# Kernel tuning notes

Measured on AMD Instinct MI355X. Metric: run time of the kernel, lower is better.

Reference implementation:

```python
import jax, jax.numpy as jnp
import numpy as np

X_SIZE, Y_SIZE, C_SIZE, H = 4, 2, 3, 128
B, C_CTX, T = 4, 512, 512


def _xavier(key, shape):
    fan_in, fan_out = shape[0], shape[1]
    a = jnp.sqrt(6.0 / (fan_in + fan_out))
    return jax.random.uniform(key, shape, jnp.float32, -a, a)


def setup_inputs() -> dict:
    key = jax.random.key(0)
    ks = jax.random.split(key, 9)
    return {
        "context_x": jax.random.normal(ks[0], (B, C_CTX, X_SIZE), jnp.float32),
        "context_y": jax.random.normal(ks[1], (B, C_CTX, Y_SIZE), jnp.float32),
        "target_x": jax.random.normal(ks[2], (B, T, X_SIZE), jnp.float32),
        "W_in": _xavier(ks[3], (C_SIZE + Y_SIZE, H)),
        "b_in": jnp.zeros((H,), jnp.float32),
        "W_ctx": _xavier(ks[4], (C_SIZE, H)),
        "b_ctx": jnp.zeros((H,), jnp.float32),
        "W_tgt": _xavier(ks[5], (H, H)),
        "b_tgt": jnp.zeros((H,), jnp.float32),
    }


def reference(context_x, context_y, target_x, W_in, b_in, W_ctx, b_ctx, W_tgt, b_tgt):
    ctx_c = context_x[..., :C_SIZE]                         # [B, C, c]
    # value: projected concat of context coords + context values
    enc_in = jnp.concatenate([ctx_c, context_y], axis=-1)   # [B, C, c+y]
    value = enc_in @ W_in + b_in                            # [B, C, H]
    key_ = ctx_c @ W_ctx + b_ctx                            # [B, C, H]
    query = target_x[..., :C_SIZE] @ W_ctx + b_ctx          # [B, T, H]
    # L1-distance attention scores: -sum_h |0.5*(key - query)|
    diff = (key_[:, None, :, :] - query[:, :, None, :]) * 0.5  # [B, T, C, H]
    scores = -jnp.sum(jnp.abs(diff), axis=-1)               # [B, T, C]
    w = jax.nn.softmax(scores, axis=-1)                     # [B, T, C]
    rep = jnp.einsum('btc,bch->bth', w, value)              # [B, T, H]
    return rep @ W_tgt + b_tgt
```

## Files before the change

### kernel.cpp

```cpp
#include <hip/hip_runtime.h>

#define BB 4
#define CC 512
#define TDIM 512
#define HH 128
#define TT 4
#define CHK 128
#define NCHK 4

__global__ __launch_bounds__(128) void prep_kernel(
    const float* __restrict__ ctx_x, const float* __restrict__ ctx_y,
    const float* __restrict__ tgt_x,
    const float* __restrict__ W_in, const float* __restrict__ b_in,
    const float* __restrict__ W_ctx, const float* __restrict__ b_ctx,
    float* __restrict__ key, float* __restrict__ query, float* __restrict__ value)
{
    int row = blockIdx.x;
    int h   = threadIdx.x;

    float4 cx = ((const float4*)ctx_x)[row];
    float2 cy = ((const float2*)ctx_y)[row];
    float4 tx = ((const float4*)tgt_x)[row];

    float wi0 = W_in[0*HH+h], wi1 = W_in[1*HH+h], wi2 = W_in[2*HH+h];
    float wi3 = W_in[3*HH+h], wi4 = W_in[4*HH+h];
    float wc0 = W_ctx[0*HH+h], wc1 = W_ctx[1*HH+h], wc2 = W_ctx[2*HH+h];
    float bi  = b_in[h], bc = b_ctx[h];

    value[row*HH+h] = fmaf(cx.x,wi0, fmaf(cx.y,wi1, fmaf(cx.z,wi2, fmaf(cy.x,wi3, fmaf(cy.y,wi4, bi)))));
    key  [row*HH+h] = fmaf(cx.x,wc0, fmaf(cx.y,wc1, fmaf(cx.z,wc2, bc)));
    query[row*HH+h] = fmaf(tx.x,wc0, fmaf(tx.y,wc1, fmaf(tx.z,wc2, bc)));
}

__global__ __launch_bounds__(256) void fused_kernel(
    const float* __restrict__ key, const float* __restrict__ query,
    const float* __restrict__ value, const float* __restrict__ W_tgt,
    const float* __restrict__ b_tgt, float* __restrict__ out)
{
    const int bx   = blockIdx.x;
    const int b    = bx >> 7;
    const int t0   = (bx & 127) * TT;
    const int tid  = threadIdx.x;
    const int g    = tid >> 6;
    const int lane = tid & 63;

    __shared__ __align__(16) float s[2][TT][CHK];
    __shared__ __align__(16) float pT[2][CHK][TT];
    __shared__ __align__(16) float fct[2][TT];
    __shared__ __align__(16) float linv[TT];
    __shared__ __align__(16) float partial[8][TT][HH];
    __shared__ __align__(16) float rep[TT][HH];

    const int cq = tid >> 3;
    const int hq = tid & 7;
    float4 qr[TT][4];
    #pragma unroll
    for (int t = 0; t < TT; ++t)
        #pragma unroll
        for (int j = 0; j < 4; ++j)
            qr[t][j] = *(const float4*)&query[(b*TDIM + t0 + t)*HH + j*32 + hq*4];

    const int cs = lane >> 5;
    const int hv = lane & 31;
    float4 acc[TT];
    #pragma unroll
    for (int t = 0; t < TT; ++t) acc[t] = make_float4(0.f,0.f,0.f,0.f);
    float m_run = -1e30f, l_run = 0.f;

    auto SCORE = [&](int ch, int p) {
        const float* kp = &key[(b*CC + ch*CHK + cq*4)*HH];
        float a0[TT], a1[TT], a2[TT], a3[TT];
        #pragma unroll
        for (int t = 0; t < TT; ++t) { a0[t]=0.f; a1[t]=0.f; a2[t]=0.f; a3[t]=0.f; }
        #pragma unroll
        for (int j = 0; j < 4; ++j) {
            const int hb = j*32 + hq*4;
            float4 k0 = *(const float4*)(kp + 0*HH + hb);
            float4 k1 = *(const float4*)(kp + 1*HH + hb);
            float4 k2 = *(const float4*)(kp + 2*HH + hb);
            float4 k3 = *(const float4*)(kp + 3*HH + hb);
            #pragma unroll
            for (int t = 0; t < TT; ++t) {
                float4 qv = qr[t][j];
                a0[t] += fabsf(k0.x-qv.x)+fabsf(k0.y-qv.y)+fabsf(k0.z-qv.z)+fabsf(k0.w-qv.w);
                a1[t] += fabsf(k1.x-qv.x)+fabsf(k1.y-qv.y)+fabsf(k1.z-qv.z)+fabsf(k1.w-qv.w);
                a2[t] += fabsf(k2.x-qv.x)+fabsf(k2.y-qv.y)+fabsf(k2.z-qv.z)+fabsf(k2.w-qv.w);
                a3[t] += fabsf(k3.x-qv.x)+fabsf(k3.y-qv.y)+fabsf(k3.z-qv.z)+fabsf(k3.w-qv.w);
            }
        }
        #pragma unroll
        for (int t = 0; t < TT; ++t) {
            float v0=a0[t], v1=a1[t], v2=a2[t], v3=a3[t];
            v0 += __shfl_xor(v0,1); v0 += __shfl_xor(v0,2); v0 += __shfl_xor(v0,4);
            v1 += __shfl_xor(v1,1); v1 += __shfl_xor(v1,2); v1 += __shfl_xor(v1,4);
            v2 += __shfl_xor(v2,1); v2 += __shfl_xor(v2,2); v2 += __shfl_xor(v2,4);
            v3 += __shfl_xor(v3,1); v3 += __shfl_xor(v3,2); v3 += __shfl_xor(v3,4);
            if (hq == 0)
                *(float4*)&s[p][t][cq*4] =
                    make_float4(-0.5f*v0, -0.5f*v1, -0.5f*v2, -0.5f*v3);
        }
    };

    auto SOFTMAX = [&](int p) {
        float x0 = s[p][g][lane], x1 = s[p][g][lane+64];
        float mc = fmaxf(x0, x1);
        #pragma unroll
        for (int msk = 32; msk; msk >>= 1) mc = fmaxf(mc, __shfl_xor(mc, msk));
        float m_new = fmaxf(m_run, mc);
        float e0 = __expf(x0 - m_new), e1 = __expf(x1 - m_new);
        float sum = e0 + e1;
        #pragma unroll
        for (int msk = 32; msk; msk >>= 1) sum += __shfl_xor(sum, msk);
        float f = __expf(m_run - m_new);
        l_run = fmaf(l_run, f, sum);
        m_run = m_new;
        pT[p][lane   ][g] = e0;
        pT[p][lane+64][g] = e1;
        if (lane == 0) fct[p][g] = f;
    };

    auto PV = [&](int ch, int p) {
        const float4 fv = *(const float4*)&fct[p][0];
        acc[0].x*=fv.x; acc[0].y*=fv.x; acc[0].z*=fv.x; acc[0].w*=fv.x;
        acc[1].x*=fv.y; acc[1].y*=fv.y; acc[1].z*=fv.y; acc[1].w*=fv.y;
        acc[2].x*=fv.z; acc[2].y*=fv.z; acc[2].z*=fv.z; acc[2].w*=fv.z;
        acc[3].x*=fv.w; acc[3].y*=fv.w; acc[3].z*=fv.w; acc[3].w*=fv.w;
        const int cbase = g*32 + cs*16;
        const float* vp = &value[(b*CC + ch*CHK + cbase)*HH + hv*4];
        #pragma unroll 4
        for (int c = 0; c < 16; ++c) {
            float4 p4 = *(const float4*)&pT[p][cbase + c][0];
            float4 vv = *(const float4*)(vp + c*HH);
            acc[0].x=fmaf(p4.x,vv.x,acc[0].x); acc[0].y=fmaf(p4.x,vv.y,acc[0].y);
            acc[0].z=fmaf(p4.x,vv.z,acc[0].z); acc[0].w=fmaf(p4.x,vv.w,acc[0].w);
            acc[1].x=fmaf(p4.y,vv.x,acc[1].x); acc[1].y=fmaf(p4.y,vv.y,acc[1].y);
            acc[1].z=fmaf(p4.y,vv.z,acc[1].z); acc[1].w=fmaf(p4.y,vv.w,acc[1].w);
            acc[2].x=fmaf(p4.z,vv.x,acc[2].x); acc[2].y=fmaf(p4.z,vv.y,acc[2].y);
            acc[2].z=fmaf(p4.z,vv.z,acc[2].z); acc[2].w=fmaf(p4.z,vv.w,acc[2].w);
            acc[3].x=fmaf(p4.w,vv.x,acc[3].x); acc[3].y=fmaf(p4.w,vv.y,acc[3].y);
            acc[3].z=fmaf(p4.w,vv.z,acc[3].z); acc[3].w=fmaf(p4.w,vv.w,acc[3].w);
        }
    };

    SCORE(0, 0);
    __syncthreads();
    SOFTMAX(0);
    __syncthreads();
    SCORE(1, 1);  PV(0, 0);
    __syncthreads();
    SOFTMAX(1);
    __syncthreads();
    SCORE(2, 0);  PV(1, 1);
    __syncthreads();
    SOFTMAX(0);
    __syncthreads();
    SCORE(3, 1);  PV(2, 0);
    __syncthreads();
    SOFTMAX(1);
    __syncthreads();
    PV(3, 1);

    if (lane == 0) linv[g] = 1.f / l_run;
    #pragma unroll
    for (int t = 0; t < TT; ++t)
        *(float4*)&partial[g*2 + cs][t][hv*4] = acc[t];
    __syncthreads();

    for (int i = tid; i < TT*HH; i += 256) {
        const int t = i >> 7, h = i & 127;
        float r = 0.f;
        #pragma unroll
        for (int gg = 0; gg < 8; ++gg) r += partial[gg][t][h];
        rep[t][h] = r * linv[t];
    }
    __syncthreads();

    {
        const int lt = tid >> 7, h = tid & 127;
        float o0 = b_tgt[h], o1 = o0;
        for (int k = 0; k < HH; k += 4) {
            float4 r0 = *(const float4*)&rep[lt    ][k];
            float4 r1 = *(const float4*)&rep[lt + 2][k];
            float w0 = W_tgt[(k+0)*HH + h];
            float w1 = W_tgt[(k+1)*HH + h];
            float w2 = W_tgt[(k+2)*HH + h];
            float w3 = W_tgt[(k+3)*HH + h];
            o0 = fmaf(r0.x,w0, fmaf(r0.y,w1, fmaf(r0.z,w2, fmaf(r0.w,w3, o0))));
            o1 = fmaf(r1.x,w0, fmaf(r1.y,w1, fmaf(r1.z,w2, fmaf(r1.w,w3, o1))));
        }
        out[(b*TDIM + t0 + lt    )*HH + h] = o0;
        out[(b*TDIM + t0 + lt + 2)*HH + h] = o1;
    }
}

extern "C" void kernel_launch(void* const* d_in, const int* in_sizes, int n_in,
                              void* d_out, int out_size, void* d_ws, size_t ws_size,
                              hipStream_t stream) {
    const float* ctx_x = (const float*)d_in[0];
    const float* ctx_y = (const float*)d_in[1];
    const float* tgt_x = (const float*)d_in[2];
    const float* W_in  = (const float*)d_in[3];
    const float* b_in  = (const float*)d_in[4];
    const float* W_ctx = (const float*)d_in[5];
    const float* b_ctx = (const float*)d_in[6];
    const float* W_tgt = (const float*)d_in[7];
    const float* b_tgt = (const float*)d_in[8];

    float* ws    = (float*)d_ws;
    float* key   = ws;
    float* query = ws + 1*BB*CC*HH;
    float* value = ws + 2*BB*CC*HH;

    prep_kernel<<<BB*CC, 128, 0, stream>>>(ctx_x, ctx_y, tgt_x,
                                           W_in, b_in, W_ctx, b_ctx,
                                           key, query, value);
    fused_kernel<<<BB*(TDIM/TT), 256, 0, stream>>>(key, query, value,
                                                   W_tgt, b_tgt, (float*)d_out);
}
```

Baseline: 35.98 us.

## Double fused attention block to 512 threads with halved per-thread work

```diff
diff --git a/kernel.cpp b/kernel.cpp
--- a/kernel.cpp
+++ b/kernel.cpp
@@ -32,7 +32,7 @@
     query[row*HH+h] = fmaf(tx.x,wc0, fmaf(tx.y,wc1, fmaf(tx.z,wc2, bc)));
 }
 
-__global__ __launch_bounds__(256) void fused_kernel(
+__global__ __launch_bounds__(512, 4) void fused_kernel(
     const float* __restrict__ key, const float* __restrict__ query,
     const float* __restrict__ value, const float* __restrict__ W_tgt,
     const float* __restrict__ b_tgt, float* __restrict__ out)
@@ -41,7 +41,7 @@
     const int b    = bx >> 7;
     const int t0   = (bx & 127) * TT;
     const int tid  = threadIdx.x;
-    const int g    = tid >> 6;
+    const int wave = tid >> 6;
     const int lane = tid & 63;
 
     __shared__ __align__(16) float s[2][TT][CHK];
@@ -51,20 +51,18 @@
     __shared__ __align__(16) float partial[8][TT][HH];
     __shared__ __align__(16) float rep[TT][HH];
 
-    const int cq = tid >> 3;
-    const int hq = tid & 7;
-    float4 qr[TT][4];
+    const int cq = tid >> 4;
+    const int hq = tid & 15;
+    float2 qr[TT][4];
     #pragma unroll
     for (int t = 0; t < TT; ++t)
         #pragma unroll
         for (int j = 0; j < 4; ++j)
-            qr[t][j] = *(const float4*)&query[(b*TDIM + t0 + t)*HH + j*32 + hq*4];
-
-    const int cs = lane >> 5;
-    const int hv = lane & 31;
-    float4 acc[TT];
+            qr[t][j] = *(const float2*)&query[(b*TDIM + t0 + t)*HH + j*32 + hq*2];
+
+    float2 acc[TT];
     #pragma unroll
-    for (int t = 0; t < TT; ++t) acc[t] = make_float4(0.f,0.f,0.f,0.f);
+    for (int t = 0; t < TT; ++t) acc[t] = make_float2(0.f, 0.f);
     float m_run = -1e30f, l_run = 0.f;
 
     auto SCORE = [&](int ch, int p) {
@@ -74,27 +72,27 @@
         for (int t = 0; t < TT; ++t) { a0[t]=0.f; a1[t]=0.f; a2[t]=0.f; a3[t]=0.f; }
         #pragma unroll
         for (int j = 0; j < 4; ++j) {
-            const int hb = j*32 + hq*4;
-            float4 k0 = *(const float4*)(kp + 0*HH + hb);
-            float4 k1 = *(const float4*)(kp + 1*HH + hb);
-            float4 k2 = *(const float4*)(kp + 2*HH + hb);
-            float4 k3 = *(const float4*)(kp + 3*HH + hb);
+            const int hb = j*32 + hq*2;
+            float2 k0 = *(const float2*)(kp + 0*HH + hb);
+            float2 k1 = *(const float2*)(kp + 1*HH + hb);
+            float2 k2 = *(const float2*)(kp + 2*HH + hb);
+            float2 k3 = *(const float2*)(kp + 3*HH + hb);
             #pragma unroll
             for (int t = 0; t < TT; ++t) {
-                float4 qv = qr[t][j];
-                a0[t] += fabsf(k0.x-qv.x)+fabsf(k0.y-qv.y)+fabsf(k0.z-qv.z)+fabsf(k0.w-qv.w);
-                a1[t] += fabsf(k1.x-qv.x)+fabsf(k1.y-qv.y)+fabsf(k1.z-qv.z)+fabsf(k1.w-qv.w);
-                a2[t] += fabsf(k2.x-qv.x)+fabsf(k2.y-qv.y)+fabsf(k2.z-qv.z)+fabsf(k2.w-qv.w);
-                a3[t] += fabsf(k3.x-qv.x)+fabsf(k3.y-qv.y)+fabsf(k3.z-qv.z)+fabsf(k3.w-qv.w);
+                float2 qv = qr[t][j];
+                a0[t] += fabsf(k0.x-qv.x) + fabsf(k0.y-qv.y);
+                a1[t] += fabsf(k1.x-qv.x) + fabsf(k1.y-qv.y);
+                a2[t] += fabsf(k2.x-qv.x) + fabsf(k2.y-qv.y);
+                a3[t] += fabsf(k3.x-qv.x) + fabsf(k3.y-qv.y);
             }
         }
         #pragma unroll
         for (int t = 0; t < TT; ++t) {
             float v0=a0[t], v1=a1[t], v2=a2[t], v3=a3[t];
-            v0 += __shfl_xor(v0,1); v0 += __shfl_xor(v0,2); v0 += __shfl_xor(v0,4);
-            v1 += __shfl_xor(v1,1); v1 += __shfl_xor(v1,2); v1 += __shfl_xor(v1,4);
-            v2 += __shfl_xor(v2,1); v2 += __shfl_xor(v2,2); v2 += __shfl_xor(v2,4);
-            v3 += __shfl_xor(v3,1); v3 += __shfl_xor(v3,2); v3 += __shfl_xor(v3,4);
+            v0 += __shfl_xor(v0,1); v0 += __shfl_xor(v0,2); v0 += __shfl_xor(v0,4); v0 += __shfl_xor(v0,8);
+            v1 += __shfl_xor(v1,1); v1 += __shfl_xor(v1,2); v1 += __shfl_xor(v1,4); v1 += __shfl_xor(v1,8);
+            v2 += __shfl_xor(v2,1); v2 += __shfl_xor(v2,2); v2 += __shfl_xor(v2,4); v2 += __shfl_xor(v2,8);
+            v3 += __shfl_xor(v3,1); v3 += __shfl_xor(v3,2); v3 += __shfl_xor(v3,4); v3 += __shfl_xor(v3,8);
             if (hq == 0)
                 *(float4*)&s[p][t][cq*4] =
                     make_float4(-0.5f*v0, -0.5f*v1, -0.5f*v2, -0.5f*v3);
@@ -102,7 +100,7 @@
     };
 
     auto SOFTMAX = [&](int p) {
-        float x0 = s[p][g][lane], x1 = s[p][g][lane+64];
+        float x0 = s[p][wave][lane], x1 = s[p][wave][lane+64];
         float mc = fmaxf(x0, x1);
         #pragma unroll
         for (int msk = 32; msk; msk >>= 1) mc = fmaxf(mc, __shfl_xor(mc, msk));
@@ -114,60 +112,56 @@
         float f = __expf(m_run - m_new);
         l_run = fmaf(l_run, f, sum);
         m_run = m_new;
-        pT[p][lane   ][g] = e0;
-        pT[p][lane+64][g] = e1;
-        if (lane == 0) fct[p][g] = f;
+        pT[p][lane   ][wave] = e0;
+        pT[p][lane+64][wave] = e1;
+        if (lane == 0) fct[p][wave] = f;
     };
 
     auto PV = [&](int ch, int p) {
         const float4 fv = *(const float4*)&fct[p][0];
-        acc[0].x*=fv.x; acc[0].y*=fv.x; acc[0].z*=fv.x; acc[0].w*=fv.x;
-        acc[1].x*=fv.y; acc[1].y*=fv.y; acc[1].z*=fv.y; acc[1].w*=fv.y;
-        acc[2].x*=fv.z; acc[2].y*=fv.z; acc[2].z*=fv.z; acc[2].w*=fv.z;
-        acc[3].x*=fv.w; acc[3].y*=fv.w; acc[3].z*=fv.w; acc[3].w*=fv.w;
-        const int cbase = g*32 + cs*16;
-        const float* vp = &value[(b*CC + ch*CHK + cbase)*HH + hv*4];
+        acc[0].x *= fv.x; acc[0].y *= fv.x;
+        acc[1].x *= fv.y; acc[1].y *= fv.y;
+        acc[2].x *= fv.z; acc[2].y *= fv.z;
+        acc[3].x *= fv.w; acc[3].y *= fv.w;
+        const int cbase = wave * 16;
+        const float* vp = &value[(b*CC + ch*CHK + cbase)*HH + lane*2];
         #pragma unroll 4
         for (int c = 0; c < 16; ++c) {
             float4 p4 = *(const float4*)&pT[p][cbase + c][0];
-            float4 vv = *(const float4*)(vp + c*HH);
-            acc[0].x=fmaf(p4.x,vv.x,acc[0].x); acc[0].y=fmaf(p4.x,vv.y,acc[0].y);
-            acc[0].z=fmaf(p4.x,vv.z,acc[0].z); acc[0].w=fmaf(p4.x,vv.w,acc[0].w);
-            acc[1].x=fmaf(p4.y,vv.x,acc[1].x); acc[1].y=fmaf(p4.y,vv.y,acc[1].y);
-            acc[1].z=fmaf(p4.y,vv.z,acc[1].z); acc[1].w=fmaf(p4.y,vv.w,acc[1].w);
-            acc[2].x=fmaf(p4.z,vv.x,acc[2].x); acc[2].y=fmaf(p4.z,vv.y,acc[2].y);
-            acc[2].z=fmaf(p4.z,vv.z,acc[2].z); acc[2].w=fmaf(p4.z,vv.w,acc[2].w);
-            acc[3].x=fmaf(p4.w,vv.x,acc[3].x); acc[3].y=fmaf(p4.w,vv.y,acc[3].y);
-            acc[3].z=fmaf(p4.w,vv.z,acc[3].z); acc[3].w=fmaf(p4.w,vv.w,acc[3].w);
+            float2 vv = *(const float2*)(vp + c*HH);
+            acc[0].x = fmaf(p4.x, vv.x, acc[0].x); acc[0].y = fmaf(p4.x, vv.y, acc[0].y);
+            acc[1].x = fmaf(p4.y, vv.x, acc[1].x); acc[1].y = fmaf(p4.y, vv.y, acc[1].y);
+            acc[2].x = fmaf(p4.z, vv.x, acc[2].x); acc[2].y = fmaf(p4.z, vv.y, acc[2].y);
+            acc[3].x = fmaf(p4.w, vv.x, acc[3].x); acc[3].y = fmaf(p4.w, vv.y, acc[3].y);
         }
     };
 
     SCORE(0, 0);
     __syncthreads();
-    SOFTMAX(0);
+    if (wave < 4) SOFTMAX(0);
     __syncthreads();
     SCORE(1, 1);  PV(0, 0);
     __syncthreads();
-    SOFTMAX(1);
+    if (wave < 4) SOFTMAX(1);
     __syncthreads();
     SCORE(2, 0);  PV(1, 1);
     __syncthreads();
-    SOFTMAX(0);
+    if (wave < 4) SOFTMAX(0);
     __syncthreads();
     SCORE(3, 1);  PV(2, 0);
     __syncthreads();
-    SOFTMAX(1);
+    if (wave < 4) SOFTMAX(1);
     __syncthreads();
     PV(3, 1);
 
-    if (lane == 0) linv[g] = 1.f / l_run;
+    if (wave < 4 && lane == 0) linv[wave] = 1.f / l_run;
     #pragma unroll
     for (int t = 0; t < TT; ++t)
-        *(float4*)&partial[g*2 + cs][t][hv*4] = acc[t];
-    __syncthreads();
-
-    for (int i = tid; i < TT*HH; i += 256) {
-        const int t = i >> 7, h = i & 127;
+        *(float2*)&partial[wave][t][lane*2] = acc[t];
+    __syncthreads();
+
+    {
+        const int t = tid >> 7, h = tid & 127;
         float r = 0.f;
         #pragma unroll
         for (int gg = 0; gg < 8; ++gg) r += partial[gg][t][h];
@@ -177,19 +171,16 @@
 
     {
         const int lt = tid >> 7, h = tid & 127;
-        float o0 = b_tgt[h], o1 = o0;
+        float o = b_tgt[h];
         for (int k = 0; k < HH; k += 4) {
-            float4 r0 = *(const float4*)&rep[lt    ][k];
-            float4 r1 = *(const float4*)&rep[lt + 2][k];
+            float4 r0 = *(const float4*)&rep[lt][k];
             float w0 = W_tgt[(k+0)*HH + h];
             float w1 = W_tgt[(k+1)*HH + h];
             float w2 = W_tgt[(k+2)*HH + h];
             float w3 = W_tgt[(k+3)*HH + h];
-            o0 = fmaf(r0.x,w0, fmaf(r0.y,w1, fmaf(r0.z,w2, fmaf(r0.w,w3, o0))));
-            o1 = fmaf(r1.x,w0, fmaf(r1.y,w1, fmaf(r1.z,w2, fmaf(r1.w,w3, o1))));
-        }
-        out[(b*TDIM + t0 + lt    )*HH + h] = o0;
-        out[(b*TDIM + t0 + lt + 2)*HH + h] = o1;
+            o = fmaf(r0.x,w0, fmaf(r0.y,w1, fmaf(r0.z,w2, fmaf(r0.w,w3, o))));
+        }
+        out[(b*TDIM + t0 + lt)*HH + h] = o;
     }
 }
 
@@ -214,6 +205,6 @@
     prep_kernel<<<BB*CC, 128, 0, stream>>>(ctx_x, ctx_y, tgt_x,
                                            W_in, b_in, W_ctx, b_ctx,
                                            key, query, value);
-    fused_kernel<<<BB*(TDIM/TT), 256, 0, stream>>>(key, query, value,
+    fused_kernel<<<BB*(TDIM/TT), 512, 0, stream>>>(key, query, value,
                                                    W_tgt, b_tgt, (float*)d_out);
 }
```

Result: slower. 48.01 us (+33.4%).

## Split context across waves with per-wave online softmax and final merge

Applied to the files above, without the earlier changes.

```diff
diff --git a/kernel.cpp b/kernel.cpp
--- a/kernel.cpp
+++ b/kernel.cpp
@@ -5,8 +5,10 @@
 #define TDIM 512
 #define HH 128
 #define TT 4
-#define CHK 128
-#define NCHK 4
+#define NW 4
+#define CPW 128
+#define SC 32
+#define NSC 4
 
 __global__ __launch_bounds__(128) void prep_kernel(
     const float* __restrict__ ctx_x, const float* __restrict__ ctx_y,
@@ -41,18 +43,18 @@
     const int b    = bx >> 7;
     const int t0   = (bx & 127) * TT;
     const int tid  = threadIdx.x;
-    const int g    = tid >> 6;
+    const int wv   = tid >> 6;
     const int lane = tid & 63;
 
-    __shared__ __align__(16) float s[2][TT][CHK];
-    __shared__ __align__(16) float pT[2][CHK][TT];
-    __shared__ __align__(16) float fct[2][TT];
-    __shared__ __align__(16) float linv[TT];
-    __shared__ __align__(16) float partial[8][TT][HH];
+    __shared__ __align__(16) float s_w[NW][TT][SC];
+    __shared__ __align__(16) float pT_w[NW][SC][TT];
+    __shared__ __align__(16) float f_w[NW][TT];
+    __shared__ __align__(16) float2 ml_w[NW][TT];
+    __shared__ __align__(16) float partial[NW][TT][HH];
     __shared__ __align__(16) float rep[TT][HH];
 
-    const int cq = tid >> 3;
-    const int hq = tid & 7;
+    const int cl = lane >> 3;
+    const int hq = lane & 7;
     float4 qr[TT][4];
     #pragma unroll
     for (int t = 0; t < TT; ++t)
@@ -60,118 +62,123 @@
         for (int j = 0; j < 4; ++j)
             qr[t][j] = *(const float4*)&query[(b*TDIM + t0 + t)*HH + j*32 + hq*4];
 
+    const int tg = lane >> 4;
+    const int ci = lane & 15;
     const int cs = lane >> 5;
     const int hv = lane & 31;
+
     float4 acc[TT];
     #pragma unroll
     for (int t = 0; t < TT; ++t) acc[t] = make_float4(0.f,0.f,0.f,0.f);
     float m_run = -1e30f, l_run = 0.f;
 
-    auto SCORE = [&](int ch, int p) {
-        const float* kp = &key[(b*CC + ch*CHK + cq*4)*HH];
-        float a0[TT], a1[TT], a2[TT], a3[TT];
-        #pragma unroll
-        for (int t = 0; t < TT; ++t) { a0[t]=0.f; a1[t]=0.f; a2[t]=0.f; a3[t]=0.f; }
-        #pragma unroll
-        for (int j = 0; j < 4; ++j) {
-            const int hb = j*32 + hq*4;
-            float4 k0 = *(const float4*)(kp + 0*HH + hb);
-            float4 k1 = *(const float4*)(kp + 1*HH + hb);
-            float4 k2 = *(const float4*)(kp + 2*HH + hb);
-            float4 k3 = *(const float4*)(kp + 3*HH + hb);
+    #pragma unroll 1
+    for (int scix = 0; scix < NSC; ++scix) {
+        const int cbase = wv*CPW + scix*SC;
+
+        {
+            const float* kp = &key[(b*CC + cbase + cl*4)*HH];
+            float a0[TT], a1[TT], a2[TT], a3[TT];
+            #pragma unroll
+            for (int t = 0; t < TT; ++t) { a0[t]=0.f; a1[t]=0.f; a2[t]=0.f; a3[t]=0.f; }
+            #pragma unroll
+            for (int j = 0; j < 4; ++j) {
+                const int hb = j*32 + hq*4;
+                float4 k0 = *(const float4*)(kp + 0*HH + hb);
+                float4 k1 = *(const float4*)(kp + 1*HH + hb);
+                float4 k2 = *(const float4*)(kp + 2*HH + hb);
+                float4 k3 = *(const float4*)(kp + 3*HH + hb);
+                #pragma unroll
+                for (int t = 0; t < TT; ++t) {
+                    float4 qv = qr[t][j];
+                    a0[t] += fabsf(k0.x-qv.x)+fabsf(k0.y-qv.y)+fabsf(k0.z-qv.z)+fabsf(k0.w-qv.w);
+                    a1[t] += fabsf(k1.x-qv.x)+fabsf(k1.y-qv.y)+fabsf(k1.z-qv.z)+fabsf(k1.w-qv.w);
+                    a2[t] += fabsf(k2.x-qv.x)+fabsf(k2.y-qv.y)+fabsf(k2.z-qv.z)+fabsf(k2.w-qv.w);
+                    a3[t] += fabsf(k3.x-qv.x)+fabsf(k3.y-qv.y)+fabsf(k3.z-qv.z)+fabsf(k3.w-qv.w);
+                }
+            }
             #pragma unroll
             for (int t = 0; t < TT; ++t) {
-                float4 qv = qr[t][j];
-                a0[t] += fabsf(k0.x-qv.x)+fabsf(k0.y-qv.y)+fabsf(k0.z-qv.z)+fabsf(k0.w-qv.w);
-                a1[t] += fabsf(k1.x-qv.x)+fabsf(k1.y-qv.y)+fabsf(k1.z-qv.z)+fabsf(k1.w-qv.w);
-                a2[t] += fabsf(k2.x-qv.x)+fabsf(k2.y-qv.y)+fabsf(k2.z-qv.z)+fabsf(k2.w-qv.w);
-                a3[t] += fabsf(k3.x-qv.x)+fabsf(k3.y-qv.y)+fabsf(k3.z-qv.z)+fabsf(k3.w-qv.w);
+                float v0=a0[t], v1=a1[t], v2=a2[t], v3=a3[t];
+                v0 += __shfl_xor(v0,1); v0 += __shfl_xor(v0,2); v0 += __shfl_xor(v0,4);
+                v1 += __shfl_xor(v1,1); v1 += __shfl_xor(v1,2); v1 += __shfl_xor(v1,4);
+                v2 += __shfl_xor(v2,1); v2 += __shfl_xor(v2,2); v2 += __shfl_xor(v2,4);
+                v3 += __shfl_xor(v3,1); v3 += __shfl_xor(v3,2); v3 += __shfl_xor(v3,4);
+                if (hq == 0)
+                    *(float4*)&s_w[wv][t][cl*4] =
+                        make_float4(-0.5f*v0, -0.5f*v1, -0.5f*v2, -0.5f*v3);
             }
         }
+
+        {
+            float x0 = s_w[wv][tg][ci*2], x1 = s_w[wv][tg][ci*2+1];
+            float mc = fmaxf(x0, x1);
+            mc = fmaxf(mc, __shfl_xor(mc,1)); mc = fmaxf(mc, __shfl_xor(mc,2));
+            mc = fmaxf(mc, __shfl_xor(mc,4)); mc = fmaxf(mc, __shfl_xor(mc,8));
+            float m_new = fmaxf(m_run, mc);
+            float e0 = __expf(x0 - m_new), e1 = __expf(x1 - m_new);
+            float sm = e0 + e1;
+            sm += __shfl_xor(sm,1); sm += __shfl_xor(sm,2);
+            sm += __shfl_xor(sm,4); sm += __shfl_xor(sm,8);
+            float f = __expf(m_run - m_new);
+            l_run = fmaf(l_run, f, sm);
+            m_run = m_new;
+            pT_w[wv][ci*2  ][tg] = e0;
+            pT_w[wv][ci*2+1][tg] = e1;
+            if (ci == 0) f_w[wv][tg] = f;
+        }
+
+        {
+            const float4 fv = *(const float4*)&f_w[wv][0];
+            acc[0].x*=fv.x; acc[0].y*=fv.x; acc[0].z*=fv.x; acc[0].w*=fv.x;
+            acc[1].x*=fv.y; acc[1].y*=fv.y; acc[1].z*=fv.y; acc[1].w*=fv.y;
+            acc[2].x*=fv.z; acc[2].y*=fv.z; acc[2].z*=fv.z; acc[2].w*=fv.z;
+            acc[3].x*=fv.w; acc[3].y*=fv.w; acc[3].z*=fv.w; acc[3].w*=fv.w;
+            const float* vp = &value[(b*CC + cbase + cs*16)*HH + hv*4];
+            #pragma unroll 4
+            for (int i = 0; i < 16; ++i) {
+                float4 p4 = *(const float4*)&pT_w[wv][cs*16 + i][0];
+                float4 vv = *(const float4*)(vp + i*HH);
+                acc[0].x=fmaf(p4.x,vv.x,acc[0].x); acc[0].y=fmaf(p4.x,vv.y,acc[0].y);
+                acc[0].z=fmaf(p4.x,vv.z,acc[0].z); acc[0].w=fmaf(p4.x,vv.w,acc[0].w);
+                acc[1].x=fmaf(p4.y,vv.x,acc[1].x); acc[1].y=fmaf(p4.y,vv.y,acc[1].y);
+                acc[1].z=fmaf(p4.y,vv.z,acc[1].z); acc[1].w=fmaf(p4.y,vv.w,acc[1].w);
+                acc[2].x=fmaf(p4.z,vv.x,acc[2].x); acc[2].y=fmaf(p4.z,vv.y,acc[2].y);
+                acc[2].z=fmaf(p4.z,vv.z,acc[2].z); acc[2].w=fmaf(p4.z,vv.w,acc[2].w);
+                acc[3].x=fmaf(p4.w,vv.x,acc[3].x); acc[3].y=fmaf(p4.w,vv.y,acc[3].y);
+                acc[3].z=fmaf(p4.w,vv.z,acc[3].z); acc[3].w=fmaf(p4.w,vv.w,acc[3].w);
+            }
+        }
+    }
+
+    #pragma unroll
+    for (int t = 0; t < TT; ++t) {
+        acc[t].x += __shfl_xor(acc[t].x, 32);
+        acc[t].y += __shfl_xor(acc[t].y, 32);
+        acc[t].z += __shfl_xor(acc[t].z, 32);
+        acc[t].w += __shfl_xor(acc[t].w, 32);
+    }
+    if (cs == 0) {
         #pragma unroll
-        for (int t = 0; t < TT; ++t) {
-            float v0=a0[t], v1=a1[t], v2=a2[t], v3=a3[t];
-            v0 += __shfl_xor(v0,1); v0 += __shfl_xor(v0,2); v0 += __shfl_xor(v0,4);
-            v1 += __shfl_xor(v1,1); v1 += __shfl_xor(v1,2); v1 += __shfl_xor(v1,4);
-            v2 += __shfl_xor(v2,1); v2 += __shfl_xor(v2,2); v2 += __shfl_xor(v2,4);
-            v3 += __shfl_xor(v3,1); v3 += __shfl_xor(v3,2); v3 += __shfl_xor(v3,4);
-            if (hq == 0)
-                *(float4*)&s[p][t][cq*4] =
-                    make_float4(-0.5f*v0, -0.5f*v1, -0.5f*v2, -0.5f*v3);
-        }
-    };
-
-    auto SOFTMAX = [&](int p) {
-        float x0 = s[p][g][lane], x1 = s[p][g][lane+64];
-        float mc = fmaxf(x0, x1);
-        #pragma unroll
-        for (int msk = 32; msk; msk >>= 1) mc = fmaxf(mc, __shfl_xor(mc, msk));
-        float m_new = fmaxf(m_run, mc);
-        float e0 = __expf(x0 - m_new), e1 = __expf(x1 - m_new);
-        float sum = e0 + e1;
-        #pragma unroll
-        for (int msk = 32; msk; msk >>= 1) sum += __shfl_xor(sum, msk);
-        float f = __expf(m_run - m_new);
-        l_run = fmaf(l_run, f, sum);
-        m_run = m_new;
-        pT[p][lane   ][g] = e0;
-        pT[p][lane+64][g] = e1;
-        if (lane == 0) fct[p][g] = f;
-    };
-
-    auto PV = [&](int ch, int p) {
-        const float4 fv = *(const float4*)&fct[p][0];
-        acc[0].x*=fv.x; acc[0].y*=fv.x; acc[0].z*=fv.x; acc[0].w*=fv.x;
-        acc[1].x*=fv.y; acc[1].y*=fv.y; acc[1].z*=fv.y; acc[1].w*=fv.y;
-        acc[2].x*=fv.z; acc[2].y*=fv.z; acc[2].z*=fv.z; acc[2].w*=fv.z;
-        acc[3].x*=fv.w; acc[3].y*=fv.w; acc[3].z*=fv.w; acc[3].w*=fv.w;
-        const int cbase = g*32 + cs*16;
-        const float* vp = &value[(b*CC + ch*CHK + cbase)*HH + hv*4];
-        #pragma unroll 4
-        for (int c = 0; c < 16; ++c) {
-            float4 p4 = *(const float4*)&pT[p][cbase + c][0];
-            float4 vv = *(const float4*)(vp + c*HH);
-            acc[0].x=fmaf(p4.x,vv.x,acc[0].x); acc[0].y=fmaf(p4.x,vv.y,acc[0].y);
-            acc[0].z=fmaf(p4.x,vv.z,acc[0].z); acc[0].w=fmaf(p4.x,vv.w,acc[0].w);
-            acc[1].x=fmaf(p4.y,vv.x,acc[1].x); acc[1].y=fmaf(p4.y,vv.y,acc[1].y);
-            acc[1].z=fmaf(p4.y,vv.z,acc[1].z); acc[1].w=fmaf(p4.y,vv.w,acc[1].w);
-            acc[2].x=fmaf(p4.z,vv.x,acc[2].x); acc[2].y=fmaf(p4.z,vv.y,acc[2].y);
-            acc[2].z=fmaf(p4.z,vv.z,acc[2].z); acc[2].w=fmaf(p4.z,vv.w,acc[2].w);
-            acc[3].x=fmaf(p4.w,vv.x,acc[3].x); acc[3].y=fmaf(p4.w,vv.y,acc[3].y);
-            acc[3].z=fmaf(p4.w,vv.z,acc[3].z); acc[3].w=fmaf(p4.w,vv.w,acc[3].w);
-        }
-    };
-
-    SCORE(0, 0);
+        for (int t = 0; t < TT; ++t)
+            *(float4*)&partial[wv][t][hv*4] = acc[t];
+    }
+    if (ci == 0) ml_w[wv][tg] = make_float2(m_run, l_run);
     __syncthreads();
-    SOFTMAX(0);
-    __syncthreads();
-    SCORE(1, 1);  PV(0, 0);
-    __syncthreads();
-    SOFTMAX(1);
-    __syncthreads();
-    SCORE(2, 0);  PV(1, 1);
-    __syncthreads();
-    SOFTMAX(0);
-    __syncthreads();
-    SCORE(3, 1);  PV(2, 0);
-    __syncthreads();
-    SOFTMAX(1);
-    __syncthreads();
-    PV(3, 1);
-
-    if (lane == 0) linv[g] = 1.f / l_run;
-    #pragma unroll
-    for (int t = 0; t < TT; ++t)
-        *(float4*)&partial[g*2 + cs][t][hv*4] = acc[t];
-    __syncthreads();
-
-    for (int i = tid; i < TT*HH; i += 256) {
-        const int t = i >> 7, h = i & 127;
-        float r = 0.f;
-        #pragma unroll
-        for (int gg = 0; gg < 8; ++gg) r += partial[gg][t][h];
-        rep[t][h] = r * linv[t];
+
+    for (int e = tid; e < TT*HH; e += 256) {
+        const int t = e >> 7, h = e & 127;
+        float mw0 = ml_w[0][t].x, lw0 = ml_w[0][t].y;
+        float mw1 = ml_w[1][t].x, lw1 = ml_w[1][t].y;
+        float mw2 = ml_w[2][t].x, lw2 = ml_w[2][t].y;
+        float mw3 = ml_w[3][t].x, lw3 = ml_w[3][t].y;
+        float M = fmaxf(fmaxf(mw0, mw1), fmaxf(mw2, mw3));
+        float a0 = __expf(mw0-M), a1 = __expf(mw1-M);
+        float a2 = __expf(mw2-M), a3 = __expf(mw3-M);
+        float L = fmaf(a0,lw0, fmaf(a1,lw1, fmaf(a2,lw2, a3*lw3)));
+        float r = a0*partial[0][t][h] + a1*partial[1][t][h]
+                + a2*partial[2][t][h] + a3*partial[3][t][h];
+        rep[t][h] = r / L;
     }
     __syncthreads();
 
```

Result: no change. 36.37 us (+1.1%).
